# Optimization experiments

Hardware: AMD Instinct MI355X
Metric: run time of the kernel (lower is better)

Reference implementation:

```python
import jax, jax.numpy as jnp
import numpy as np

D_MODEL = 1024
NUM_HEADS = 16
D_K = D_MODEL // NUM_HEADS
ROPE_THETA = 10000.0
SEQ = 4096


def setup_inputs() -> dict:
    key = jax.random.key(0)
    ks = jax.random.split(key, 5)
    s = 1.0 / np.sqrt(D_MODEL)
    return {
        "x": jax.random.normal(ks[0], (1, SEQ, D_MODEL), jnp.float32),
        "token_positions": jnp.arange(SEQ, dtype=jnp.int32),
        "Wq": jax.random.normal(ks[1], (D_MODEL, D_MODEL), jnp.float32) * s,
        "Wk": jax.random.normal(ks[2], (D_MODEL, D_MODEL), jnp.float32) * s,
        "Wv": jax.random.normal(ks[3], (D_MODEL, D_MODEL), jnp.float32) * s,
        "Wo": jax.random.normal(ks[4], (D_MODEL, D_MODEL), jnp.float32) * s,
    }


def _rope(t, positions):
    # t: [b, h, s, d_k]; interleaved pair rotation
    half = D_K // 2
    inv_freq = ROPE_THETA ** (-jnp.arange(half, dtype=jnp.float32) * 2.0 / D_K)
    ang = positions.astype(jnp.float32)[:, None] * inv_freq[None, :]  # [s, half]
    cos, sin = jnp.cos(ang), jnp.sin(ang)
    x1 = t[..., 0::2]
    x2 = t[..., 1::2]
    r1 = x1 * cos - x2 * sin
    r2 = x1 * sin + x2 * cos
    return jnp.stack([r1, r2], axis=-1).reshape(t.shape)


def reference(x, token_positions, Wq, Wk, Wv, Wo):
    b, s, _ = x.shape
    def split_heads(t):
        return t.reshape(b, s, NUM_HEADS, D_K).transpose(0, 2, 1, 3)  # [b,h,s,dk]
    q = split_heads(x @ Wq.T)
    k = split_heads(x @ Wk.T)
    v = split_heads(x @ Wv.T)
    q = _rope(q, token_positions)
    k = _rope(k, token_positions)
    scores = jnp.einsum('bhqd,bhkd->bhqk', q, k) / np.sqrt(D_K)
    causal = jnp.tril(jnp.ones((s, s), dtype=bool))
    scores = jnp.where(causal, scores, -jnp.inf)
    attn = jax.nn.softmax(scores, axis=-1)
    out = jnp.einsum('bhqk,bhkd->bhqd', attn, v)
    out = out.transpose(0, 2, 1, 3).reshape(b, s, D_MODEL)
    return out @ Wo.T
```

## Files before the change

kernel.cpp:

```cpp
#include <hip/hip_runtime.h>

#define S    4096
#define DM   1024
#define H    16
#define DK   64

typedef __bf16 bf16;
typedef __bf16 bf16x8 __attribute__((ext_vector_type(8)));
typedef __bf16 bf16x4 __attribute__((ext_vector_type(4)));
typedef float  f32x4  __attribute__((ext_vector_type(4)));

__global__ __launch_bounds__(256)
void convert_kernel(const float* __restrict__ x,  const float* __restrict__ wq,
                    const float* __restrict__ wk, const float* __restrict__ wv,
                    const float* __restrict__ wo,
                    bf16* __restrict__ xb,  bf16* __restrict__ wqb,
                    bf16* __restrict__ wkb, bf16* __restrict__ wvb,
                    bf16* __restrict__ wob)
{
    const size_t i = (size_t)blockIdx.x * 256 + threadIdx.x;
    const float* src; bf16* dst; size_t off;
    if (i < 1048576)      { src = x;  dst = xb;  off = i; }
    else if (i < 1310720) { src = wq; dst = wqb; off = i - 1048576; }
    else if (i < 1572864) { src = wk; dst = wkb; off = i - 1310720; }
    else if (i < 1835008) { src = wv; dst = wvb; off = i - 1572864; }
    else                  { src = wo; dst = wob; off = i - 1835008; }
    f32x4 v = ((const f32x4*)src)[off];
    bf16x4 b;
    for (int r = 0; r < 4; r++) b[r] = (bf16)v[r];
    ((bf16x4*)dst)[off] = b;
}

__global__ __launch_bounds__(256)
void gemm_kernel(const bf16* __restrict__ A,
                 const bf16* __restrict__ w0, const bf16* __restrict__ w1,
                 const bf16* __restrict__ w2,
                 const int* __restrict__ pos,
                 bf16* __restrict__ o0, bf16* __restrict__ o1,
                 bf16* __restrict__ o2,
                 float* __restrict__ of,
                 int base_mode)
{
    const int z    = blockIdx.z;
    const int mode = base_mode + z;
    const bf16* W  = (z == 0) ? w0 : (z == 1 ? w1 : w2);
    bf16* Out      = (z == 0) ? o0 : (z == 1 ? o1 : o2);

    __shared__ bf16 As[64 * 72];
    __shared__ bf16 Bs[64 * 72];

    const int tid  = threadIdx.x;
    const int lane = tid & 63;
    const int wv   = tid >> 6;
    const int quad = lane >> 4;
    const int col  = lane & 15;
    const int wm   = wv >> 1, wn = wv & 1;

    const int tileM = blockIdx.x * 64;
    const int tileN = blockIdx.y * 64;

    const int ldRow = tid >> 2;
    const int ldK   = (tid & 3) * 16;

    f32x4 acc[2][2] = {};

    for (int kc = 0; kc < DM; kc += 64) {
        bf16x8 a0 = *(const bf16x8*)&A[(size_t)(tileM + ldRow) * DM + kc + ldK];
        bf16x8 a1 = *(const bf16x8*)&A[(size_t)(tileM + ldRow) * DM + kc + ldK + 8];
        bf16x8 b0 = *(const bf16x8*)&W[(size_t)(tileN + ldRow) * DM + kc + ldK];
        bf16x8 b1 = *(const bf16x8*)&W[(size_t)(tileN + ldRow) * DM + kc + ldK + 8];
        __syncthreads();
        *(bf16x8*)&As[ldRow * 72 + ldK]     = a0;
        *(bf16x8*)&As[ldRow * 72 + ldK + 8] = a1;
        *(bf16x8*)&Bs[ldRow * 72 + ldK]     = b0;
        *(bf16x8*)&Bs[ldRow * 72 + ldK + 8] = b1;
        __syncthreads();

        for (int kk = 0; kk < 2; kk++) {
            bf16x8 af0 = *(const bf16x8*)&As[(wm * 32 + 0 * 16 + col) * 72 + kk * 32 + quad * 8];
            bf16x8 af1 = *(const bf16x8*)&As[(wm * 32 + 1 * 16 + col) * 72 + kk * 32 + quad * 8];
            bf16x8 bf0 = *(const bf16x8*)&Bs[(wn * 32 + 0 * 16 + col) * 72 + kk * 32 + quad * 8];
            bf16x8 bf1 = *(const bf16x8*)&Bs[(wn * 32 + 1 * 16 + col) * 72 + kk * 32 + quad * 8];

            acc[0][0] = __builtin_amdgcn_mfma_f32_16x16x32_bf16(af0, bf0, acc[0][0], 0, 0, 0);
            acc[0][1] = __builtin_amdgcn_mfma_f32_16x16x32_bf16(af0, bf1, acc[0][1], 0, 0, 0);
            acc[1][0] = __builtin_amdgcn_mfma_f32_16x16x32_bf16(af1, bf0, acc[1][0], 0, 0, 0);
            acc[1][1] = __builtin_amdgcn_mfma_f32_16x16x32_bf16(af1, bf1, acc[1][1], 0, 0, 0);
        }
    }

    for (int fm = 0; fm < 2; fm++)
    for (int fn = 0; fn < 2; fn++) {
        f32x4 v = acc[fm][fn];
        const int n = tileN + wn * 32 + fn * 16 + col;
        for (int r = 0; r < 4; r++) {
            const int m = tileM + wm * 32 + fm * 16 + quad * 4 + r;
            float val = v[r];
            if (mode <= 1) {
                float part = __shfl_xor(val, 1);
                const int d = n & 63;
                const int i = d >> 1;
                float inv = exp2f(-(float)i * 0.41524101186092034f);
                float ang = (float)pos[m] * inv;
                float c = cosf(ang), sn = sinf(ang);
                float rot = (n & 1) ? (val * c + part * sn)
                                    : (val * c - part * sn);
                if (mode == 0) rot *= 0.18033688011112042f;
                Out[((size_t)(n >> 6) * S + m) * 64 + d] = (bf16)rot;
            } else if (mode == 2) {
                Out[(size_t)n * S + m] = (bf16)val;
            } else {
                of[(size_t)m * DM + n] = val;
            }
        }
    }
}

__global__ __launch_bounds__(256, 3)
void attn_kernel(const bf16* __restrict__ q, const bf16* __restrict__ k,
                 const bf16* __restrict__ vt, bf16* __restrict__ ao)
{
    const int bx   = blockIdx.x;
    const int qb_  = (bx & 1) ? (63 - (bx >> 1)) : (bx >> 1);
    const int h    = blockIdx.y;
    const int tid  = threadIdx.x;
    const int lane = tid & 63;
    const int wv   = tid >> 6;
    const int quad = lane >> 4;
    const int col  = lane & 15;

    __shared__ bf16 Ks[64 * 72];
    __shared__ bf16 Vs[64 * 72];
    __shared__ bf16 plds[4][16 * 72];

    const int qbase = qb_ * 64 + wv * 16;

    bf16x8 qf0 = *(const bf16x8*)&q[((size_t)(h * S + qbase + col)) * 64 + quad * 8];
    bf16x8 qf1 = *(const bf16x8*)&q[((size_t)(h * S + qbase + col)) * 64 + 32 + quad * 8];

    float li = 0.f;
    f32x4 o[4] = {};
    const int gq = qbase + col;

    const int srow = tid >> 2;
    const int sseg = (tid & 3) * 16;
    const bf16* kg_ = k  + ((size_t)h * S) * 64;
    const bf16* vg_ = vt + ((size_t)h * 64) * S;

    bf16x8 kr0 = *(const bf16x8*)(kg_ + (size_t)srow * 64 + sseg);
    bf16x8 kr1 = *(const bf16x8*)(kg_ + (size_t)srow * 64 + sseg + 8);
    bf16x8 vr0 = *(const bf16x8*)(vg_ + (size_t)srow * S + sseg);
    bf16x8 vr1 = *(const bf16x8*)(vg_ + (size_t)srow * S + sseg + 8);

    for (int kt = 0; kt <= qb_; kt++) {
        const int kbase = kt * 64;

        __syncthreads();
        *(bf16x8*)&Ks[srow * 72 + sseg]     = kr0;
        *(bf16x8*)&Ks[srow * 72 + sseg + 8] = kr1;
        *(bf16x8*)&Vs[srow * 72 + sseg]     = vr0;
        *(bf16x8*)&Vs[srow * 72 + sseg + 8] = vr1;
        __syncthreads();

        if (kt < qb_) {
            const int nb = kbase + 64;
            kr0 = *(const bf16x8*)(kg_ + (size_t)(nb + srow) * 64 + sseg);
            kr1 = *(const bf16x8*)(kg_ + (size_t)(nb + srow) * 64 + sseg + 8);
            vr0 = *(const bf16x8*)(vg_ + (size_t)srow * S + nb + sseg);
            vr1 = *(const bf16x8*)(vg_ + (size_t)srow * S + nb + sseg + 8);
        }

        f32x4 st[4];
        for (int kg = 0; kg < 4; kg++) {
            bf16x8 kf0 = *(const bf16x8*)&Ks[(kg * 16 + col) * 72 + quad * 8];
            bf16x8 kf1 = *(const bf16x8*)&Ks[(kg * 16 + col) * 72 + 32 + quad * 8];
            f32x4 zz = {};
            zz = __builtin_amdgcn_mfma_f32_16x16x32_bf16(kf0, qf0, zz, 0, 0, 0);
            zz = __builtin_amdgcn_mfma_f32_16x16x32_bf16(kf1, qf1, zz, 0, 0, 0);
            st[kg] = zz;
        }

        if (kt == qb_) {
            for (int kg = 0; kg < 4; kg++)
                for (int r = 0; r < 4; r++) {
                    const int gk = kbase + kg * 16 + quad * 4 + r;
                    st[kg][r] = (gk > gq) ? -1e30f : st[kg][r];
                }
        }

        float ps = 0.f;
        for (int kg = 0; kg < 4; kg++) {
            bf16x4 pk;
            for (int r = 0; r < 4; r++) {
                float p = exp2f(st[kg][r]);
                ps += p;
                pk[r] = (bf16)p;
            }
            *(bf16x4*)&plds[wv][col * 72 + kg * 16 + quad * 4] = pk;
        }
        ps += __shfl_xor(ps, 16);
        ps += __shfl_xor(ps, 32);
        li += ps;

        __builtin_amdgcn_wave_barrier();

        bf16x8 pb0 = *(const bf16x8*)&plds[wv][col * 72 + quad * 8];
        bf16x8 pb1 = *(const bf16x8*)&plds[wv][col * 72 + 32 + quad * 8];

        for (int dg = 0; dg < 4; dg++) {
            bf16x8 va0 = *(const bf16x8*)&Vs[(dg * 16 + col) * 72 + quad * 8];
            bf16x8 va1 = *(const bf16x8*)&Vs[(dg * 16 + col) * 72 + 32 + quad * 8];
            o[dg] = __builtin_amdgcn_mfma_f32_16x16x32_bf16(va0, pb0, o[dg], 0, 0, 0);
            o[dg] = __builtin_amdgcn_mfma_f32_16x16x32_bf16(va1, pb1, o[dg], 0, 0, 0);
        }
    }

    const float rli = 1.f / li;
    for (int dg = 0; dg < 4; dg++) {
        bf16x4 ov;
        for (int r = 0; r < 4; r++) ov[r] = (bf16)(o[dg][r] * rli);
        *(bf16x4*)&ao[(size_t)(qbase + col) * DM + h * 64 + dg * 16 + quad * 4] = ov;
    }
}

extern "C" void kernel_launch(void* const* d_in, const int* in_sizes, int n_in,
                              void* d_out, int out_size, void* d_ws, size_t ws_size,
                              hipStream_t stream)
{
    const float* x   = (const float*)d_in[0];
    const int*   pos = (const int*)d_in[1];
    const float* Wq  = (const float*)d_in[2];
    const float* Wk  = (const float*)d_in[3];
    const float* Wv  = (const float*)d_in[4];
    const float* Wo  = (const float*)d_in[5];
    float* out = (float*)d_out;

    char* w = (char*)d_ws;
    bf16* xb  = (bf16*)(w);
    bf16* wqb = (bf16*)(w + (size_t) 8 * 1024 * 1024);
    bf16* wkb = (bf16*)(w + (size_t)10 * 1024 * 1024);
    bf16* wvb = (bf16*)(w + (size_t)12 * 1024 * 1024);
    bf16* wob = (bf16*)(w + (size_t)14 * 1024 * 1024);
    bf16* qb  = (bf16*)(w + (size_t)16 * 1024 * 1024);
    bf16* kb  = (bf16*)(w + (size_t)24 * 1024 * 1024);
    bf16* vt  = (bf16*)(w + (size_t)32 * 1024 * 1024);
    bf16* ao  = (bf16*)(w + (size_t)40 * 1024 * 1024);

    dim3 blk(256);
    convert_kernel<<<dim3(8192), blk, 0, stream>>>(x, Wq, Wk, Wv, Wo,
                                                   xb, wqb, wkb, wvb, wob);
    gemm_kernel<<<dim3(64, 16, 3), blk, 0, stream>>>(xb, wqb, wkb, wvb, pos,
                                                     qb, kb, vt, out, 0);
    attn_kernel<<<dim3(64, 16), blk, 0, stream>>>(qb, kb, vt, ao);
    gemm_kernel<<<dim3(64, 16, 1), blk, 0, stream>>>(ao, wob, wob, wob, pos,
                                                     qb, kb, vt, out, 3);
}
```

Before: 283.4 us.

## Split attention KV range across two blocks and combine partial outputs

The causal attention loop over key tiles is split in two halves along a new grid z dimension. Each half writes unnormalized bf16 partial outputs and row sums, and a new combine kernel adds them and normalizes. The aim is more blocks, better load balance on the long causal rows and higher occupancy (launch bounds raised to 5). MFMA sections are also wrapped in s_setprio. This costs an extra kernel launch, extra global traffic for the partials, and bf16 rounding of the unnormalized partials. Workspace buffers are reused by aliasing the freed x and weight regions.

```diff
diff --git a/kernel.cpp b/kernel.cpp
--- a/kernel.cpp
+++ b/kernel.cpp
@@ -116,19 +116,27 @@
     }
 }
 
-__global__ __launch_bounds__(256, 3)
+__global__ __launch_bounds__(256, 5)
 void attn_kernel(const bf16* __restrict__ q, const bf16* __restrict__ k,
-                 const bf16* __restrict__ vt, bf16* __restrict__ ao)
+                 const bf16* __restrict__ vt,
+                 bf16* __restrict__ P0g, bf16* __restrict__ P1g,
+                 float* __restrict__ l0g, float* __restrict__ l1g)
 {
     const int bx   = blockIdx.x;
     const int qb_  = (bx & 1) ? (63 - (bx >> 1)) : (bx >> 1);
     const int h    = blockIdx.y;
+    const int z    = blockIdx.z;
     const int tid  = threadIdx.x;
     const int lane = tid & 63;
     const int wv   = tid >> 6;
     const int quad = lane >> 4;
     const int col  = lane & 15;
 
+    const int nt   = qb_ + 1;
+    const int half = (nt + 1) >> 1;
+    const int kt0  = z ? half : 0;
+    const int kt1  = z ? nt   : half;
+
     __shared__ bf16 Ks[64 * 72];
     __shared__ bf16 Vs[64 * 72];
     __shared__ bf16 plds[4][16 * 72];
@@ -147,12 +155,12 @@
     const bf16* kg_ = k  + ((size_t)h * S) * 64;
     const bf16* vg_ = vt + ((size_t)h * 64) * S;
 
-    bf16x8 kr0 = *(const bf16x8*)(kg_ + (size_t)srow * 64 + sseg);
-    bf16x8 kr1 = *(const bf16x8*)(kg_ + (size_t)srow * 64 + sseg + 8);
-    bf16x8 vr0 = *(const bf16x8*)(vg_ + (size_t)srow * S + sseg);
-    bf16x8 vr1 = *(const bf16x8*)(vg_ + (size_t)srow * S + sseg + 8);
-
-    for (int kt = 0; kt <= qb_; kt++) {
+    bf16x8 kr0 = *(const bf16x8*)(kg_ + (size_t)(kt0 * 64 + srow) * 64 + sseg);
+    bf16x8 kr1 = *(const bf16x8*)(kg_ + (size_t)(kt0 * 64 + srow) * 64 + sseg + 8);
+    bf16x8 vr0 = *(const bf16x8*)(vg_ + (size_t)srow * S + kt0 * 64 + sseg);
+    bf16x8 vr1 = *(const bf16x8*)(vg_ + (size_t)srow * S + kt0 * 64 + sseg + 8);
+
+    for (int kt = kt0; kt < kt1; kt++) {
         const int kbase = kt * 64;
 
         __syncthreads();
@@ -162,7 +170,7 @@
         *(bf16x8*)&Vs[srow * 72 + sseg + 8] = vr1;
         __syncthreads();
 
-        if (kt < qb_) {
+        if (kt + 1 < kt1) {
             const int nb = kbase + 64;
             kr0 = *(const bf16x8*)(kg_ + (size_t)(nb + srow) * 64 + sseg);
             kr1 = *(const bf16x8*)(kg_ + (size_t)(nb + srow) * 64 + sseg + 8);
@@ -171,6 +179,7 @@
         }
 
         f32x4 st[4];
+        __builtin_amdgcn_s_setprio(1);
         for (int kg = 0; kg < 4; kg++) {
             bf16x8 kf0 = *(const bf16x8*)&Ks[(kg * 16 + col) * 72 + quad * 8];
             bf16x8 kf1 = *(const bf16x8*)&Ks[(kg * 16 + col) * 72 + 32 + quad * 8];
@@ -179,6 +188,7 @@
             zz = __builtin_amdgcn_mfma_f32_16x16x32_bf16(kf1, qf1, zz, 0, 0, 0);
             st[kg] = zz;
         }
+        __builtin_amdgcn_s_setprio(0);
 
         if (kt == qb_) {
             for (int kg = 0; kg < 4; kg++)
@@ -207,20 +217,43 @@
         bf16x8 pb0 = *(const bf16x8*)&plds[wv][col * 72 + quad * 8];
         bf16x8 pb1 = *(const bf16x8*)&plds[wv][col * 72 + 32 + quad * 8];
 
+        __builtin_amdgcn_s_setprio(1);
         for (int dg = 0; dg < 4; dg++) {
             bf16x8 va0 = *(const bf16x8*)&Vs[(dg * 16 + col) * 72 + quad * 8];
             bf16x8 va1 = *(const bf16x8*)&Vs[(dg * 16 + col) * 72 + 32 + quad * 8];
             o[dg] = __builtin_amdgcn_mfma_f32_16x16x32_bf16(va0, pb0, o[dg], 0, 0, 0);
             o[dg] = __builtin_amdgcn_mfma_f32_16x16x32_bf16(va1, pb1, o[dg], 0, 0, 0);
         }
-    }
-
-    const float rli = 1.f / li;
+        __builtin_amdgcn_s_setprio(0);
+    }
+
+    bf16*  Pz = z ? P1g : P0g;
+    float* lz = z ? l1g : l0g;
     for (int dg = 0; dg < 4; dg++) {
         bf16x4 ov;
-        for (int r = 0; r < 4; r++) ov[r] = (bf16)(o[dg][r] * rli);
-        *(bf16x4*)&ao[(size_t)(qbase + col) * DM + h * 64 + dg * 16 + quad * 4] = ov;
-    }
+        for (int r = 0; r < 4; r++) ov[r] = (bf16)o[dg][r];
+        *(bf16x4*)&Pz[(size_t)gq * DM + h * 64 + dg * 16 + quad * 4] = ov;
+    }
+    if (quad == 0) lz[(size_t)h * S + gq] = li;
+}
+
+__global__ __launch_bounds__(256)
+void combine_kernel(const bf16* __restrict__ P0, const bf16* __restrict__ P1,
+                    const float* __restrict__ l0, const float* __restrict__ l1,
+                    bf16* __restrict__ ao)
+{
+    const size_t i    = (size_t)blockIdx.x * 256 + threadIdx.x;
+    const size_t base = i * 8;
+    const int s  = (int)(base >> 10);
+    const int dm = (int)(base & 1023);
+    const int h  = dm >> 6;
+    const float rli = 1.f / (l0[(size_t)h * S + s] + l1[(size_t)h * S + s]);
+    bf16x8 a = *(const bf16x8*)&P0[base];
+    bf16x8 b = *(const bf16x8*)&P1[base];
+    bf16x8 ov;
+    for (int r = 0; r < 8; r++)
+        ov[r] = (bf16)(((float)a[r] + (float)b[r]) * rli);
+    *(bf16x8*)&ao[base] = ov;
 }
 
 extern "C" void kernel_launch(void* const* d_in, const int* in_sizes, int n_in,
@@ -236,22 +269,28 @@
     float* out = (float*)d_out;
 
     char* w = (char*)d_ws;
-    bf16* xb  = (bf16*)(w);
-    bf16* wqb = (bf16*)(w + (size_t) 8 * 1024 * 1024);
-    bf16* wkb = (bf16*)(w + (size_t)10 * 1024 * 1024);
-    bf16* wvb = (bf16*)(w + (size_t)12 * 1024 * 1024);
-    bf16* wob = (bf16*)(w + (size_t)14 * 1024 * 1024);
-    bf16* qb  = (bf16*)(w + (size_t)16 * 1024 * 1024);
-    bf16* kb  = (bf16*)(w + (size_t)24 * 1024 * 1024);
-    bf16* vt  = (bf16*)(w + (size_t)32 * 1024 * 1024);
-    bf16* ao  = (bf16*)(w + (size_t)40 * 1024 * 1024);
+    bf16*  xb  = (bf16*)(w);
+    bf16*  wqb = (bf16*)(w + (size_t) 8 * 1024 * 1024);
+    bf16*  wkb = (bf16*)(w + (size_t)10 * 1024 * 1024);
+    bf16*  wvb = (bf16*)(w + (size_t)12 * 1024 * 1024);
+    bf16*  P0  = (bf16*)(w);
+    bf16*  P1  = (bf16*)(w + (size_t) 8 * 1024 * 1024);
+    bf16*  qb  = (bf16*)(w + (size_t)16 * 1024 * 1024);
+    bf16*  kb  = (bf16*)(w + (size_t)24 * 1024 * 1024);
+    bf16*  vt  = (bf16*)(w + (size_t)32 * 1024 * 1024);
+    float* l0  = (float*)(w + (size_t)40 * 1024 * 1024);
+    float* l1  = (float*)(w + (size_t)40 * 1024 * 1024 + 256 * 1024);
+    bf16*  ao  = (bf16*)(w + (size_t)16 * 1024 * 1024);
+    bf16*  wob = (bf16*)(w + (size_t)46 * 1024 * 1024);
 
     dim3 blk(256);
     convert_kernel<<<dim3(8192), blk, 0, stream>>>(x, Wq, Wk, Wv, Wo,
                                                    xb, wqb, wkb, wvb, wob);
     gemm_kernel<<<dim3(64, 16, 3), blk, 0, stream>>>(xb, wqb, wkb, wvb, pos,
                                                      qb, kb, vt, out, 0);
-    attn_kernel<<<dim3(64, 16), blk, 0, stream>>>(qb, kb, vt, ao);
+    attn_kernel<<<dim3(64, 16, 2), blk, 0, stream>>>(qb, kb, vt,
+                                                     P0, P1, l0, l1);
+    combine_kernel<<<dim3(2048), blk, 0, stream>>>(P0, P1, l0, l1, ao);
     gemm_kernel<<<dim3(64, 16, 1), blk, 0, stream>>>(ao, wob, wob, wob, pos,
-                                                     qb, kb, vt, out, 3);
-}
+                                                     P0, P0, P0, out, 3);
+}
```

Measured after the change: 280.2 us. Within noise of the previous version (-1.1%).
